# Optimization experiments

Measured on AMD Instinct MI355X. Metric: run time of the kernel, lower is better.

Reference implementation:

```python
import jax, jax.numpy as jnp
import numpy as np

NUM_HEADS = 16
ROPE_BASE = 10000.0


def _rope_interleaved(x, cos, sin):
    # x: [B,S,H,Hd]; cos/sin: [S,Hd/2]. Interleaved pairs (even, odd).
    x1 = x[..., 0::2]
    x2 = x[..., 1::2]
    c = cos[None, :, None, :]
    s = sin[None, :, None, :]
    o1 = x1 * c - x2 * s
    o2 = x1 * s + x2 * c
    return jnp.stack([o1, o2], axis=-1).reshape(x.shape)


def setup_inputs() -> dict:
    key = jax.random.key(0)
    ks = jax.random.split(key, 5)
    B, S, D = 2, 2048, 2048
    init_scale = 0.02
    x = jax.random.normal(ks[0], (B, S, D), jnp.float32)
    Wq = jax.random.normal(ks[1], (D, D), jnp.float32) * init_scale
    Wk = jax.random.normal(ks[2], (D, D), jnp.float32) * init_scale
    Wv = jax.random.normal(ks[3], (D, D), jnp.float32) * init_scale
    Wo = jax.random.normal(ks[4], (D, D), jnp.float32) * init_scale
    return {"x": x, "Wq": Wq, "Wk": Wk, "Wv": Wv, "Wo": Wo}


def reference(x, Wq, Wk, Wv, Wo):
    B, S, D = x.shape
    H = NUM_HEADS
    Hd = D // H
    # QKV projections (bias-free)
    q = (x @ Wq).reshape(B, S, H, Hd)
    k = (x @ Wk).reshape(B, S, H, Hd)
    v = (x @ Wv).reshape(B, S, H, Hd)
    # Rotary embedding, interleaved, base 10000, full head_dim
    pos = jnp.arange(S, dtype=jnp.float32)
    inv_freq = 1.0 / (ROPE_BASE ** (jnp.arange(0, Hd, 2, dtype=jnp.float32) / Hd))
    angles = pos[:, None] * inv_freq[None, :]  # [S, Hd/2]
    cos, sin = jnp.cos(angles), jnp.sin(angles)
    q = _rope_interleaved(q, cos, sin)
    k = _rope_interleaved(k, cos, sin)
    # Causal scaled-dot-product attention (flash_attn_func default scale = Hd**-0.5)
    scale = Hd ** -0.5
    scores = jnp.einsum('bqhd,bkhd->bhqk', q, k) * scale
    causal = jnp.tril(jnp.ones((S, S), dtype=bool))
    scores = jnp.where(causal[None, None], scores, jnp.finfo(scores.dtype).min)
    probs = jax.nn.softmax(scores, axis=-1)
    attn = jnp.einsum('bhqk,bkhd->bqhd', probs, v).reshape(B, S, D)
    return attn @ Wo
```

## Files before the change

### kernel.cpp

```cpp
#include <hip/hip_runtime.h>
#include <hip/hip_bf16.h>

static constexpr int BB = 2;
static constexpr int SS = 2048;
static constexpr int DD = 2048;
static constexpr int HH = 16;
static constexpr int HD = 128;

typedef __bf16 bf16_t;
typedef __bf16 bf16x8 __attribute__((ext_vector_type(8)));
typedef __bf16 bf16x4 __attribute__((ext_vector_type(4)));
typedef float  floatx4 __attribute__((ext_vector_type(4)));

__device__ __forceinline__ void gl2lds16(const bf16_t* g, bf16_t* l) {
    __builtin_amdgcn_global_load_lds(
        (const __attribute__((address_space(1))) void*)g,
        (__attribute__((address_space(3))) void*)l, 16, 0, 0);
}

__global__ void cast_x_kernel(const float* __restrict__ x, bf16_t* __restrict__ xb) {
    int i = blockIdx.x * 256 + threadIdx.x;
    float4 v = ((const float4*)x)[i];
    bf16x4 o;
    o.x = (bf16_t)v.x; o.y = (bf16_t)v.y; o.z = (bf16_t)v.z; o.w = (bf16_t)v.w;
    ((bf16x4*)xb)[i] = o;
}

__global__ void transpose_cast_kernel(const float* __restrict__ W, bf16_t* __restrict__ Wt) {
    __shared__ float tile[32][33];
    int bx = blockIdx.x * 32;
    int by = blockIdx.y * 32;
    int tx = threadIdx.x, ty = threadIdx.y;
#pragma unroll
    for (int j = 0; j < 4; ++j)
        tile[ty + j * 8][tx] = W[(size_t)(by + ty + j * 8) * DD + bx + tx];
    __syncthreads();
#pragma unroll
    for (int j = 0; j < 4; ++j)
        Wt[(size_t)(bx + ty + j * 8) * DD + by + tx] = (bf16_t)tile[tx][ty + j * 8];
}

template <int MODE>
__global__ __launch_bounds__(256, 2) void gemm_bt_kernel(
    const bf16_t* __restrict__ A, const bf16_t* __restrict__ Bt,
    float* __restrict__ Cf, bf16_t* __restrict__ Qw, bf16_t* __restrict__ Kw,
    bf16_t* __restrict__ Vw, int N, int K) {
    __shared__ __align__(16) bf16_t As[128 * 64];
    __shared__ __align__(16) bf16_t Bs[128 * 64];

    const int t = threadIdx.x;
    const int lane = t & 63;
    const int wave = t >> 6;
    const int lrow = lane & 15;
    const int lkq  = lane >> 4;
    const int wm = (wave & 1) * 64;
    const int wn = (wave >> 1) * 64;
    const int m0 = blockIdx.y * 128;
    const int n0 = blockIdx.x * 128;

    floatx4 acc[4][4];
#pragma unroll
    for (int i = 0; i < 4; ++i)
#pragma unroll
        for (int j = 0; j < 4; ++j) acc[i][j] = (floatx4)0.0f;

    const int srow  = lane >> 3;
    const int sch   = (lane & 7) ^ srow;

    for (int k0 = 0; k0 < K; k0 += 64) {
        __syncthreads();
#pragma unroll
        for (int p = 0; p < 4; ++p) {
            int r = wave * 32 + p * 8 + srow;
            gl2lds16(A  + (size_t)(m0 + r) * K + k0 + sch * 8, As + (wave * 32 + p * 8) * 64);
            gl2lds16(Bt + (size_t)(n0 + r) * K + k0 + sch * 8, Bs + (wave * 32 + p * 8) * 64);
        }
        __syncthreads();
#pragma unroll
        for (int ks = 0; ks < 2; ++ks) {
            bf16x8 af[4], bg[4];
#pragma unroll
            for (int i = 0; i < 4; ++i) {
                int pos = ((ks * 4 + lkq) ^ (lrow & 7)) * 8;
                af[i] = *(const bf16x8*)(As + (wm + i * 16 + lrow) * 64 + pos);
                bg[i] = *(const bf16x8*)(Bs + (wn + i * 16 + lrow) * 64 + pos);
            }
#pragma unroll
            for (int i = 0; i < 4; ++i)
#pragma unroll
                for (int j = 0; j < 4; ++j)
                    acc[i][j] = __builtin_amdgcn_mfma_f32_16x16x32_bf16(af[i], bg[j], acc[i][j], 0, 0, 0);
        }
    }

#pragma unroll
    for (int i = 0; i < 4; ++i)
#pragma unroll
        for (int j = 0; j < 4; ++j)
#pragma unroll
            for (int r = 0; r < 4; ++r) {
                int m = m0 + wm + i * 16 + lkq * 4 + r;
                int n = n0 + wn + j * 16 + lrow;
                float v = acc[i][j][r];
                if (MODE == 1) {
                    Cf[(size_t)m * N + n] = v;
                } else {
                    bf16_t bv = (bf16_t)v;
                    int b = m >> 11, s = m & (SS - 1);
                    int nn = n & (DD - 1);
                    int h = nn >> 7, d = nn & 127;
                    size_t off = (((size_t)b * HH + h) * SS + s) * HD + d;
                    if (n < DD)            Qw[off] = bv;
                    else if (n < 2 * DD)   Kw[off] = bv;
                    else                   Vw[off] = bv;
                }
            }
}

__global__ void rope_kernel(bf16_t* __restrict__ Qw, bf16_t* __restrict__ Kw) {
    int idx = blockIdx.x * 256 + threadIdx.x;
    int i  = idx & 63;
    int s  = (idx >> 6) & (SS - 1);
    int bh = idx >> 17;
    float inv = expf(-(float)(2 * i) * (9.210340371976184f / 128.0f));
    float ang = (float)s * inv;
    float c = cosf(ang), sn = sinf(ang);
    size_t base = ((size_t)bh * SS + s) * HD + 2 * i;
    float q1 = (float)Qw[base], q2 = (float)Qw[base + 1];
    Qw[base]     = (bf16_t)(q1 * c - q2 * sn);
    Qw[base + 1] = (bf16_t)(q1 * sn + q2 * c);
    float k1 = (float)Kw[base], k2 = (float)Kw[base + 1];
    Kw[base]     = (bf16_t)(k1 * c - k2 * sn);
    Kw[base + 1] = (bf16_t)(k1 * sn + k2 * c);
}

__global__ void vtrans_kernel(const bf16_t* __restrict__ Vw, bf16_t* __restrict__ Vt) {
    __shared__ unsigned short lds[64][65];
    const int t = threadIdx.x;
    const int s0 = blockIdx.x * 64, d0 = blockIdx.y * 64, bh = blockIdx.z;
    const bf16_t* src = Vw + ((size_t)bh * SS + s0) * HD + d0;
    bf16_t* dst = Vt + ((size_t)bh * HD + d0) * SS + s0;
#pragma unroll
    for (int p = 0; p < 2; ++p) {
        int c = p * 256 + t;
        int s = c >> 3, ch = c & 7;
        uint4 v = *(const uint4*)(src + (size_t)s * HD + ch * 8);
        const unsigned short* pv = (const unsigned short*)&v;
#pragma unroll
        for (int e = 0; e < 8; ++e) lds[ch * 8 + e][s] = pv[e];
    }
    __syncthreads();
    {
        int d = t >> 2, sb = (t & 3) * 16;
        uint4 o[2];
        unsigned short* po = (unsigned short*)o;
#pragma unroll
        for (int e = 0; e < 16; ++e) {
            int p = sb + e;
            int s = (p & ~31) | ((p & 4) << 2) | ((p & 24) >> 1) | (p & 3);
            po[e] = lds[d][s];
        }
        *(uint4*)(dst + (size_t)d * SS + sb) = o[0];
        *(uint4*)(dst + (size_t)d * SS + sb + 8) = o[1];
    }
}

__global__ __launch_bounds__(256, 4) void flash_attn_kernel(
    const bf16_t* __restrict__ Qw, const bf16_t* __restrict__ Kw,
    const bf16_t* __restrict__ Vtw, bf16_t* __restrict__ Attn) {
    __shared__ __align__(16) bf16_t Ks[64 * 128];
    __shared__ __align__(16) bf16_t Vs[128 * 64];

    const int t = threadIdx.x;
    const int lane = t & 63;
    const int wave = t >> 6;
    const int lrow = lane & 15;
    const int lkq  = lane >> 4;
    const int bx = blockIdx.x;
    const int qtile = (bx & 1) ? (bx >> 1) : (31 - (bx >> 1));
    const int bh = blockIdx.y;
    const int q0 = qtile * 64;

    const bf16_t* Qbh = Qw + (size_t)bh * SS * HD;
    const bf16_t* Kbh = Kw + (size_t)bh * SS * HD;
    const bf16_t* Vbh = Vtw + (size_t)bh * HD * SS;

    const int qb = q0 + wave * 16;

    const float qscale = 0.08838834764831845f * 1.4426950408889634f;
    bf16x8 qf[4];
#pragma unroll
    for (int kc4 = 0; kc4 < 4; ++kc4) {
        qf[kc4] = *(const bf16x8*)(Qbh + (size_t)(qb + lrow) * HD + kc4 * 32 + lkq * 8);
#pragma unroll
        for (int e = 0; e < 8; ++e) qf[kc4][e] = (bf16_t)((float)qf[kc4][e] * qscale);
    }

    floatx4 oacc[8];
#pragma unroll
    for (int i = 0; i < 8; ++i) oacc[i] = (floatx4)0.0f;
    float m_i = -1e30f;
    float l_i = 0.0f;

    const int nch = qtile + 1;
    for (int kc = 0; kc < nch; ++kc) {
        __syncthreads();
#pragma unroll
        for (int p = 0; p < 4; ++p) {
            int row = wave * 16 + p * 4 + (lane >> 4);
            int gch = (lane & 15) ^ (row & 7);
            gl2lds16(Kbh + (size_t)(kc * 64 + row) * HD + gch * 8,
                     Ks + (wave * 16 + p * 4) * 128);
        }
#pragma unroll
        for (int p = 0; p < 4; ++p) {
            int row = wave * 32 + p * 8 + (lane >> 3);
            int gch = (lane & 7) ^ (row & 7);
            gl2lds16(Vbh + (size_t)row * SS + kc * 64 + gch * 8,
                     Vs + (wave * 32 + p * 8) * 64);
        }
        __syncthreads();

        floatx4 sacc[4];
#pragma unroll
        for (int i = 0; i < 4; ++i) sacc[i] = (floatx4)0.0f;
#pragma unroll
        for (int nf = 0; nf < 4; ++nf)
#pragma unroll
            for (int kc4 = 0; kc4 < 4; ++kc4) {
                bf16x8 kf = *(const bf16x8*)(Ks + (nf * 16 + lrow) * 128 +
                                             (((kc4 * 4 + lkq) ^ (lrow & 7)) * 8));
                sacc[nf] = __builtin_amdgcn_mfma_f32_16x16x32_bf16(kf, qf[kc4], sacc[nf], 0, 0, 0);
            }

        const int qg = qb + lrow;
        float mx = m_i;
        if (kc == nch - 1) {
#pragma unroll
            for (int nf = 0; nf < 4; ++nf)
#pragma unroll
                for (int r = 0; r < 4; ++r) {
                    int kg = kc * 64 + nf * 16 + lkq * 4 + r;
                    float sv = (kg > qg) ? -1e30f : sacc[nf][r];
                    sacc[nf][r] = sv;
                    mx = fmaxf(mx, sv);
                }
        } else {
#pragma unroll
            for (int nf = 0; nf < 4; ++nf)
#pragma unroll
                for (int r = 0; r < 4; ++r) mx = fmaxf(mx, sacc[nf][r]);
        }
        mx = fmaxf(mx, __shfl_xor(mx, 16));
        mx = fmaxf(mx, __shfl_xor(mx, 32));
        float alpha = exp2f(m_i - mx);
        m_i = mx;

        float rs = 0.0f;
#pragma unroll
        for (int nf = 0; nf < 4; ++nf)
#pragma unroll
            for (int r = 0; r < 4; ++r) {
                float pv = exp2f(sacc[nf][r] - mx);
                sacc[nf][r] = pv;
                rs += pv;
            }
        rs += __shfl_xor(rs, 16);
        rs += __shfl_xor(rs, 32);
        l_i = l_i * alpha + rs;

        if (__ballot(alpha < 1.0f)) {
            float av[4];
#pragma unroll
            for (int r = 0; r < 4; ++r) av[r] = __shfl(alpha, lkq * 4 + r);
#pragma unroll
            for (int nf8 = 0; nf8 < 8; ++nf8)
#pragma unroll
                for (int r = 0; r < 4; ++r) oacc[nf8][r] *= av[r];
        }

        bf16x8 pa[2];
#pragma unroll
        for (int k2 = 0; k2 < 2; ++k2) {
            bf16x8 t8;
#pragma unroll
            for (int j = 0; j < 8; ++j)
                t8[j] = (bf16_t)sacc[2 * k2 + (j >> 2)][j & 3];
            pa[k2] = t8;
        }

#pragma unroll
        for (int nf8 = 0; nf8 < 8; ++nf8)
#pragma unroll
            for (int k2 = 0; k2 < 2; ++k2) {
                bf16x8 vf = *(const bf16x8*)(Vs + (nf8 * 16 + lrow) * 64 +
                                             (((k2 * 4 + lkq) ^ (lrow & 7)) * 8));
                oacc[nf8] = __builtin_amdgcn_mfma_f32_16x16x32_bf16(pa[k2], vf, oacc[nf8], 0, 0, 0);
            }
    }

    int bb = bh >> 4, h = bh & 15;
#pragma unroll
    for (int r = 0; r < 4; ++r) {
        float invl = 1.0f / __shfl(l_i, lkq * 4 + r);
        int q = qb + lkq * 4 + r;
#pragma unroll
        for (int nf8 = 0; nf8 < 8; ++nf8)
            Attn[((size_t)bb * SS + q) * DD + h * HD + nf8 * 16 + lrow] =
                (bf16_t)(oacc[nf8][r] * invl);
    }
}

extern "C" void kernel_launch(void* const* d_in, const int* in_sizes, int n_in,
                              void* d_out, int out_size, void* d_ws, size_t ws_size,
                              hipStream_t stream) {
    const float* x  = (const float*)d_in[0];
    const float* Wq = (const float*)d_in[1];
    const float* Wk = (const float*)d_in[2];
    const float* Wv = (const float*)d_in[3];
    const float* Wo = (const float*)d_in[4];
    float* out = (float*)d_out;

    bf16_t* p = (bf16_t*)d_ws;
    bf16_t* Xb    = p; p += (size_t)BB * SS * DD;
    bf16_t* Wqkvt = p; p += (size_t)3 * DD * DD;
    bf16_t* Wot   = p; p += (size_t)DD * DD;
    bf16_t* Qw    = p; p += (size_t)BB * HH * SS * HD;
    bf16_t* Kw    = p; p += (size_t)BB * HH * SS * HD;
    bf16_t* Vtw   = p; p += (size_t)BB * HH * SS * HD;
    bf16_t* Attn  = p; p += (size_t)BB * SS * DD;
    bf16_t* Vw = Attn;

    cast_x_kernel<<<(BB * SS * DD / 4) / 256, 256, 0, stream>>>(x, Xb);

    dim3 tb(32, 8), tg(DD / 32, DD / 32);
    transpose_cast_kernel<<<tg, tb, 0, stream>>>(Wq, Wqkvt);
    transpose_cast_kernel<<<tg, tb, 0, stream>>>(Wk, Wqkvt + (size_t)DD * DD);
    transpose_cast_kernel<<<tg, tb, 0, stream>>>(Wv, Wqkvt + (size_t)2 * DD * DD);
    transpose_cast_kernel<<<tg, tb, 0, stream>>>(Wo, Wot);

    gemm_bt_kernel<0><<<dim3(3 * DD / 128, BB * SS / 128), 256, 0, stream>>>(
        Xb, Wqkvt, nullptr, Qw, Kw, Vw, 3 * DD, DD);

    rope_kernel<<<(BB * HH * SS * 64) / 256, 256, 0, stream>>>(Qw, Kw);

    vtrans_kernel<<<dim3(SS / 64, HD / 64, BB * HH), 256, 0, stream>>>(Vw, Vtw);

    flash_attn_kernel<<<dim3(SS / 64, BB * HH), 256, 0, stream>>>(Qw, Kw, Vtw, Attn);

    gemm_bt_kernel<1><<<dim3(DD / 128, BB * SS / 128), 256, 0, stream>>>(
        Attn, Wot, out, nullptr, nullptr, nullptr, DD, DD);
}
```

Before: 399.3 us.

## Double-buffer K/V tiles in flash attention with async LDS prefetch

Gives K and V two LDS buffers each and prefetches the next KV chunk into the idle buffer while the current chunk is computed. Explicit vmcnt waits and raw barriers replace the two __syncthreads per iteration, so global load latency overlaps the MFMA work. LDS use doubles and launch bounds drop from 4 to 2 blocks per CU, which lowers occupancy. The hand-written vmcnt count and the missing LDS-specific waits add correctness risk.

Result: slower. 437.1 us (+9.5%).

```diff
diff --git a/kernel.cpp b/kernel.cpp
--- a/kernel.cpp
+++ b/kernel.cpp
@@ -165,11 +165,11 @@
     }
 }
 
-__global__ __launch_bounds__(256, 4) void flash_attn_kernel(
+__global__ __launch_bounds__(256, 2) void flash_attn_kernel(
     const bf16_t* __restrict__ Qw, const bf16_t* __restrict__ Kw,
     const bf16_t* __restrict__ Vtw, bf16_t* __restrict__ Attn) {
-    __shared__ __align__(16) bf16_t Ks[64 * 128];
-    __shared__ __align__(16) bf16_t Vs[128 * 64];
+    __shared__ __align__(16) bf16_t Ks[2][64 * 128];
+    __shared__ __align__(16) bf16_t Vs[2][128 * 64];
 
     const int t = threadIdx.x;
     const int lane = t & 63;
@@ -187,6 +187,11 @@
 
     const int qb = q0 + wave * 16;
 
+    const int krow = wave * 16 + (lane >> 4);
+    const int kgch = (lane & 15);
+    const int vrow = wave * 32 + (lane >> 3);
+    const int vgch = (lane & 7);
+
     const float qscale = 0.08838834764831845f * 1.4426950408889634f;
     bf16x8 qf[4];
 #pragma unroll
@@ -203,23 +208,45 @@
     float l_i = 0.0f;
 
     const int nch = qtile + 1;
+
+#pragma unroll
+    for (int p = 0; p < 4; ++p) {
+        int row = krow + p * 4;
+        gl2lds16(Kbh + (size_t)row * HD + (kgch ^ (row & 7)) * 8,
+                 Ks[0] + (wave * 16 + p * 4) * 128);
+    }
+#pragma unroll
+    for (int p = 0; p < 4; ++p) {
+        int row = vrow + p * 8;
+        gl2lds16(Vbh + (size_t)row * SS + (vgch ^ (row & 7)) * 8,
+                 Vs[0] + (wave * 32 + p * 8) * 64);
+    }
+
     for (int kc = 0; kc < nch; ++kc) {
-        __syncthreads();
-#pragma unroll
-        for (int p = 0; p < 4; ++p) {
-            int row = wave * 16 + p * 4 + (lane >> 4);
-            int gch = (lane & 15) ^ (row & 7);
-            gl2lds16(Kbh + (size_t)(kc * 64 + row) * HD + gch * 8,
-                     Ks + (wave * 16 + p * 4) * 128);
-        }
-#pragma unroll
-        for (int p = 0; p < 4; ++p) {
-            int row = wave * 32 + p * 8 + (lane >> 3);
-            int gch = (lane & 7) ^ (row & 7);
-            gl2lds16(Vbh + (size_t)row * SS + kc * 64 + gch * 8,
-                     Vs + (wave * 32 + p * 8) * 64);
-        }
-        __syncthreads();
+        const int cur = kc & 1;
+        if (kc + 1 < nch) {
+            const int nb = cur ^ 1;
+            const size_t kco = (size_t)(kc + 1) * 64;
+#pragma unroll
+            for (int p = 0; p < 4; ++p) {
+                int row = krow + p * 4;
+                gl2lds16(Kbh + (kco + row) * HD + (kgch ^ (row & 7)) * 8,
+                         Ks[nb] + (wave * 16 + p * 4) * 128);
+            }
+#pragma unroll
+            for (int p = 0; p < 4; ++p) {
+                int row = vrow + p * 8;
+                gl2lds16(Vbh + (size_t)row * SS + kco + (vgch ^ (row & 7)) * 8,
+                         Vs[nb] + (wave * 32 + p * 8) * 64);
+            }
+            asm volatile("s_waitcnt vmcnt(8)" ::: "memory");
+        } else {
+            asm volatile("s_waitcnt vmcnt(0)" ::: "memory");
+        }
+        __builtin_amdgcn_s_barrier();
+
+        const bf16_t* Ksc = Ks[cur];
+        const bf16_t* Vsc = Vs[cur];
 
         floatx4 sacc[4];
 #pragma unroll
@@ -228,7 +255,7 @@
         for (int nf = 0; nf < 4; ++nf)
 #pragma unroll
             for (int kc4 = 0; kc4 < 4; ++kc4) {
-                bf16x8 kf = *(const bf16x8*)(Ks + (nf * 16 + lrow) * 128 +
+                bf16x8 kf = *(const bf16x8*)(Ksc + (nf * 16 + lrow) * 128 +
                                              (((kc4 * 4 + lkq) ^ (lrow & 7)) * 8));
                 sacc[nf] = __builtin_amdgcn_mfma_f32_16x16x32_bf16(kf, qf[kc4], sacc[nf], 0, 0, 0);
             }
@@ -293,10 +320,12 @@
         for (int nf8 = 0; nf8 < 8; ++nf8)
 #pragma unroll
             for (int k2 = 0; k2 < 2; ++k2) {
-                bf16x8 vf = *(const bf16x8*)(Vs + (nf8 * 16 + lrow) * 64 +
+                bf16x8 vf = *(const bf16x8*)(Vsc + (nf8 * 16 + lrow) * 64 +
                                              (((k2 * 4 + lkq) ^ (lrow & 7)) * 8));
                 oacc[nf8] = __builtin_amdgcn_mfma_f32_16x16x32_bf16(pa[k2], vf, oacc[nf8], 0, 0, 0);
             }
+
+        __builtin_amdgcn_s_barrier();
     }
 
     int bb = bh >> 4, h = bh & 15;
```
